# Kernel tuning notes

Hardware: AMD Instinct MI355X
Metric: run time of the kernel (lower is better)

Reference implementation:

```python
import jax, jax.numpy as jnp
import numpy as np

N_NODES = 100000
N_EDGES = 1600000
N_GRAPHS = 256
NODE = 64
EDGE = 64
GLOB = 64
HID = 64


def _lin_init(key, fan_in, fan_out):
    kw, kb = jax.random.split(key)
    bound = 1.0 / np.sqrt(fan_in)
    W = jax.random.uniform(kw, (fan_in, fan_out), minval=-bound, maxval=bound, dtype=jnp.float32)
    b = jax.random.uniform(kb, (fan_out,), minval=-bound, maxval=bound, dtype=jnp.float32)
    return W, b


def setup_inputs() -> dict:
    key = jax.random.key(0)
    ks = jax.random.split(key, 9)
    x = jax.random.normal(ks[0], (N_NODES, NODE), dtype=jnp.float32)
    edge_index = jax.random.randint(ks[1], (2, N_EDGES), 0, N_NODES, dtype=jnp.int32)
    edge_attr = jax.random.normal(ks[2], (N_EDGES, EDGE), dtype=jnp.float32)
    u = jax.random.normal(ks[3], (N_GRAPHS, GLOB), dtype=jnp.float32)
    batch = jnp.sort(jax.random.randint(ks[4], (N_NODES,), 0, N_GRAPHS, dtype=jnp.int32))
    W1a, b1a = _lin_init(ks[5], NODE + EDGE, HID)
    W1b, b1b = _lin_init(ks[6], HID, HID)
    W2a, b2a = _lin_init(ks[7], NODE + HID + GLOB, HID)
    W2b, b2b = _lin_init(ks[8], HID, NODE)
    return {"x": x, "edge_index": edge_index, "edge_attr": edge_attr, "u": u,
            "batch": batch, "W1a": W1a, "b1a": b1a, "W1b": W1b, "b1b": b1b,
            "W2a": W2a, "b2a": b2a, "W2b": W2b, "b2b": b2b}


def reference(x, edge_index, edge_attr, u, batch, W1a, b1a, W1b, b1b, W2a, b2a, W2b, b2b):
    row, col = edge_index[0], edge_index[1]
    # gather source node feats + edge feats -> [E, node+edge]
    out = jnp.concatenate([x[row], edge_attr], axis=1)
    out = jax.nn.selu(out @ W1a + b1a) @ W1b + b1b  # node_mlp_1 -> [E, HID]
    # scatter_mean into destination nodes
    summed = jax.ops.segment_sum(out, col, num_segments=x.shape[0])
    counts = jax.ops.segment_sum(jnp.ones((out.shape[0],), out.dtype), col, num_segments=x.shape[0])
    mean = summed / jnp.maximum(counts, 1.0)[:, None]
    h = jnp.concatenate([x, mean, u[batch]], axis=1)  # [N, node+HID+glob]
    return jax.nn.selu(h @ W2a + b2a) @ W2b + b2b
```

## Files before the change

### kernel.cpp

```cpp
#include <hip/hip_runtime.h>

#define NN 100000
#define NE 1600000
#define NT_E (NE / 16)
#define NT_N ((NN + 15) / 16)

typedef __attribute__((ext_vector_type(8))) short short8;
typedef __attribute__((ext_vector_type(4))) float f32x4;

__device__ __forceinline__ short f2b(float x) {
    unsigned u = __builtin_bit_cast(unsigned, x);
    u = (u + 0x7FFFu + ((u >> 16) & 1u)) >> 16;
    return (short)u;
}
__device__ __forceinline__ float b2f(unsigned short b) {
    return __builtin_bit_cast(float, (unsigned)b << 16);
}

__device__ __forceinline__ float selu_f(float x) {
    const float scale = 1.0507009873554805f;
    const float asc   = 1.7580993408473766f;
    return x > 0.f ? scale * x : asc * (__expf(x) - 1.f);
}

__device__ __forceinline__ short8 pack8(const float* __restrict__ p) {
    const f32x4 a = *reinterpret_cast<const f32x4*>(p);
    const f32x4 b = *reinterpret_cast<const f32x4*>(p + 4);
    short8 r;
#pragma unroll
    for (int j = 0; j < 4; ++j) { r[j] = f2b(a[j]); r[j + 4] = f2b(b[j]); }
    return r;
}

__device__ __forceinline__ short8 pack8nt(const float* __restrict__ p) {
    const f32x4 a = __builtin_nontemporal_load(reinterpret_cast<const f32x4*>(p));
    const f32x4 b = __builtin_nontemporal_load(reinterpret_cast<const f32x4*>(p + 4));
    short8 r;
#pragma unroll
    for (int j = 0; j < 4; ++j) { r[j] = f2b(a[j]); r[j + 4] = f2b(b[j]); }
    return r;
}

__device__ __forceinline__ short8 ld_frag(const unsigned short* __restrict__ base, int idx, int lane) {
    return *reinterpret_cast<const short8*>(base + ((size_t)idx * 64 + lane) * 8);
}

__device__ __forceinline__ f32x4 mm(short8 a, short8 b, f32x4 c) {
    return __builtin_amdgcn_mfma_f32_16x16x32_bf16(a, b, c, 0, 0, 0);
}

__global__ void frag_setup(const float* __restrict__ W1a, const float* __restrict__ W1b,
                           const float* __restrict__ W2a, const float* __restrict__ W2b,
                           unsigned short* __restrict__ fw) {
    const int lane = threadIdx.x;
    const int p = lane & 15, q = lane >> 4;
    const int f = blockIdx.x;
    const float* W; int idx; unsigned short* dst;
    if (f < 16)      { W = W1a; idx = f;      dst = fw; }
    else if (f < 24) { W = W1b; idx = f - 16; dst = fw + 16 * 512; }
    else if (f < 48) { W = W2a; idx = f - 24; dst = fw + 24 * 512; }
    else             { W = W2b; idx = f - 48; dst = fw + 48 * 512; }
    const int t = idx >> 2, n = idx & 3;
    const float* base = W + (t * 32 + q * 8) * 64 + n * 16 + p;
    unsigned short* o = dst + ((size_t)idx * 64 + lane) * 8;
#pragma unroll
    for (int j = 0; j < 8; ++j) o[j] = (unsigned short)f2b(base[j * 64]);
}

__global__ __launch_bounds__(256) void edge_kernel(
    const float* __restrict__ x, const int* __restrict__ row, const int* __restrict__ col,
    const float* __restrict__ ea,
    const unsigned short* __restrict__ fw1a, const float* __restrict__ b1a,
    const unsigned short* __restrict__ fw1b, const float* __restrict__ b1b,
    unsigned short* __restrict__ summed, float* __restrict__ counts)
{
    __shared__ __attribute__((aligned(16))) short hlds[4][16 * 72];
    const int lane = threadIdx.x & 63;
    const int wid  = threadIdx.x >> 6;
    const int p = lane & 15, q = lane >> 4;
    short* hl = hlds[wid];

    short8 B1[4][4], B2[2][4];
#pragma unroll
    for (int t = 0; t < 4; ++t)
#pragma unroll
        for (int n = 0; n < 4; ++n) B1[t][n] = ld_frag(fw1a, t * 4 + n, lane);
#pragma unroll
    for (int t = 0; t < 2; ++t)
#pragma unroll
        for (int n = 0; n < 4; ++n) B2[t][n] = ld_frag(fw1b, t * 4 + n, lane);
    float bias1[4], bias2[4];
#pragma unroll
    for (int n = 0; n < 4; ++n) { bias1[n] = b1a[n * 16 + p]; bias2[n] = b1b[n * 16 + p]; }

    const int tstride = gridDim.x * 4;
    int tile = blockIdx.x * 4 + wid;
    int rs = (tile < NT_E) ? row[tile * 16 + p] : 0;

    for (; tile < NT_E; tile += tstride) {
        const int e = tile * 16 + p;
        const float* xr = x + (size_t)rs * 64 + q * 8;
        const float* er = ea + (size_t)e * 64 + q * 8;
        short8 a0 = pack8(xr);
        short8 a1 = pack8(xr + 32);
        short8 a2 = pack8nt(er);
        short8 a3 = pack8nt(er + 32);

        const int tn = tile + tstride;
        const int rs_next = (tn < NT_E) ? row[tn * 16 + p] : 0;

        int cd[4];
#pragma unroll
        for (int i = 0; i < 4; ++i) cd[i] = col[tile * 16 + q * 4 + i];

        f32x4 acc[4];
#pragma unroll
        for (int n = 0; n < 4; ++n) acc[n] = (f32x4){0.f, 0.f, 0.f, 0.f};
#pragma unroll
        for (int n = 0; n < 4; ++n) {
            acc[n] = mm(a0, B1[0][n], acc[n]);
            acc[n] = mm(a1, B1[1][n], acc[n]);
            acc[n] = mm(a2, B1[2][n], acc[n]);
            acc[n] = mm(a3, B1[3][n], acc[n]);
        }
#pragma unroll
        for (int n = 0; n < 4; ++n)
#pragma unroll
            for (int i = 0; i < 4; ++i)
                hl[(q * 4 + i) * 72 + n * 16 + p] = f2b(selu_f(acc[n][i] + bias1[n]));

        short8 h0 = *reinterpret_cast<const short8*>(hl + p * 72 + q * 8);
        short8 h1 = *reinterpret_cast<const short8*>(hl + p * 72 + 32 + q * 8);

        f32x4 acc2[4];
#pragma unroll
        for (int n = 0; n < 4; ++n) acc2[n] = (f32x4){0.f, 0.f, 0.f, 0.f};
#pragma unroll
        for (int n = 0; n < 4; ++n) {
            acc2[n] = mm(h0, B2[0][n], acc2[n]);
            acc2[n] = mm(h1, B2[1][n], acc2[n]);
        }

#pragma unroll
        for (int n = 0; n < 4; ++n)
#pragma unroll
            for (int i = 0; i < 4; ++i) {
                const float v = acc2[n][i] + bias2[n];
                const float o = __shfl_xor(v, 1);
                if (!(p & 1)) {
                    unsigned pk = ((unsigned)(unsigned short)f2b(o) << 16) |
                                  (unsigned)(unsigned short)f2b(v);
                    unsigned long long addr =
                        (unsigned long long)(summed + (size_t)cd[i] * 64 + n * 16 + p);
                    asm volatile("global_atomic_pk_add_bf16 %0, %1, off"
                                 :: "v"(addr), "v"(pk) : "memory");
                }
            }
        if (lane < 16) unsafeAtomicAdd(&counts[col[e]], 1.0f);
        rs = rs_next;
    }
}

__global__ __launch_bounds__(256) void node_kernel(
    const float* __restrict__ x, const float* __restrict__ u, const int* __restrict__ batch,
    const unsigned short* __restrict__ summed, const float* __restrict__ counts,
    const unsigned short* __restrict__ fw2a, const float* __restrict__ b2a,
    const unsigned short* __restrict__ fw2b, const float* __restrict__ b2b,
    float* __restrict__ out)
{
    __shared__ __attribute__((aligned(16))) short hlds[4][16 * 72];
    const int lane = threadIdx.x & 63;
    const int wid  = threadIdx.x >> 6;
    const int p = lane & 15, q = lane >> 4;
    short* hl = hlds[wid];

    short8 BA[6][4], BB[2][4];
#pragma unroll
    for (int t = 0; t < 6; ++t)
#pragma unroll
        for (int n = 0; n < 4; ++n) BA[t][n] = ld_frag(fw2a, t * 4 + n, lane);
#pragma unroll
    for (int t = 0; t < 2; ++t)
#pragma unroll
        for (int n = 0; n < 4; ++n) BB[t][n] = ld_frag(fw2b, t * 4 + n, lane);
    float bias1[4], bias2[4];
#pragma unroll
    for (int n = 0; n < 4; ++n) { bias1[n] = b2a[n * 16 + p]; bias2[n] = b2b[n * 16 + p]; }

    const int tstride = gridDim.x * 4;
    for (int tile = blockIdx.x * 4 + wid; tile < NT_N; tile += tstride) {
        const int v = tile * 16 + p;
        const float* xr = x + (size_t)v * 64 + q * 8;
        short8 a0 = pack8(xr);
        short8 a1 = pack8(xr + 32);

        const float rc = 1.f / fmaxf(counts[v], 1.f);
        const unsigned short* sr = summed + (size_t)v * 64 + q * 8;
        short8 s0 = *reinterpret_cast<const short8*>(sr);
        short8 s1 = *reinterpret_cast<const short8*>(sr + 32);
        short8 a2, a3;
#pragma unroll
        for (int j = 0; j < 8; ++j) {
            a2[j] = f2b(b2f((unsigned short)s0[j]) * rc);
            a3[j] = f2b(b2f((unsigned short)s1[j]) * rc);
        }
        const int g = batch[v];
        const float* ur = u + (size_t)g * 64 + q * 8;
        short8 a4 = pack8(ur);
        short8 a5 = pack8(ur + 32);

        f32x4 acc[4];
#pragma unroll
        for (int n = 0; n < 4; ++n) acc[n] = (f32x4){0.f, 0.f, 0.f, 0.f};
#pragma unroll
        for (int n = 0; n < 4; ++n) {
            acc[n] = mm(a0, BA[0][n], acc[n]);
            acc[n] = mm(a1, BA[1][n], acc[n]);
            acc[n] = mm(a2, BA[2][n], acc[n]);
            acc[n] = mm(a3, BA[3][n], acc[n]);
            acc[n] = mm(a4, BA[4][n], acc[n]);
            acc[n] = mm(a5, BA[5][n], acc[n]);
        }
#pragma unroll
        for (int n = 0; n < 4; ++n)
#pragma unroll
            for (int i = 0; i < 4; ++i)
                hl[(q * 4 + i) * 72 + n * 16 + p] = f2b(selu_f(acc[n][i] + bias1[n]));

        short8 h0 = *reinterpret_cast<const short8*>(hl + p * 72 + q * 8);
        short8 h1 = *reinterpret_cast<const short8*>(hl + p * 72 + 32 + q * 8);

        f32x4 acc2[4];
#pragma unroll
        for (int n = 0; n < 4; ++n) acc2[n] = (f32x4){0.f, 0.f, 0.f, 0.f};
#pragma unroll
        for (int n = 0; n < 4; ++n) {
            acc2[n] = mm(h0, BB[0][n], acc2[n]);
            acc2[n] = mm(h1, BB[1][n], acc2[n]);
        }
#pragma unroll
        for (int n = 0; n < 4; ++n)
#pragma unroll
            for (int i = 0; i < 4; ++i)
                out[((size_t)tile * 16 + q * 4 + i) * 64 + n * 16 + p] = acc2[n][i] + bias2[n];
    }
}

extern "C" void kernel_launch(void* const* d_in, const int* in_sizes, int n_in,
                              void* d_out, int out_size, void* d_ws, size_t ws_size,
                              hipStream_t stream) {
    const float* x     = (const float*)d_in[0];
    const int*   ei    = (const int*)d_in[1];
    const float* ea    = (const float*)d_in[2];
    const float* u     = (const float*)d_in[3];
    const int*   batch = (const int*)d_in[4];
    const float* W1a   = (const float*)d_in[5];
    const float* b1a   = (const float*)d_in[6];
    const float* W1b   = (const float*)d_in[7];
    const float* b1b   = (const float*)d_in[8];
    const float* W2a   = (const float*)d_in[9];
    const float* b2a   = (const float*)d_in[10];
    const float* W2b   = (const float*)d_in[11];
    const float* b2b   = (const float*)d_in[12];
    float* out = (float*)d_out;

    unsigned short* summed = (unsigned short*)d_ws;
    float* counts = (float*)((char*)d_ws + (size_t)NN * 64 * 2);
    unsigned short* fw = (unsigned short*)((char*)d_ws + 13200000);
    const unsigned short* fw1a = fw;
    const unsigned short* fw1b = fw + 16 * 512;
    const unsigned short* fw2a = fw + 24 * 512;
    const unsigned short* fw2b = fw + 48 * 512;

    hipMemsetAsync(d_ws, 0, 13200000, stream);
    frag_setup<<<56, 64, 0, stream>>>(W1a, W1b, W2a, W2b, fw);

    const int* row = ei;
    const int* col = ei + NE;
    edge_kernel<<<1024, 256, 0, stream>>>(x, row, col, ea, fw1a, b1a, fw1b, b1b, summed, counts);
    node_kernel<<<1024, 256, 0, stream>>>(x, u, batch, summed, counts, fw2a, b2a, fw2b, b2b, out);
}
```

Baseline: 908.9 us.

## Replace atomic scatter with CSR gather and move second edge linear past mean

Builds a CSR by destination node (histogram, three-pass scan, atomic scatter of edge ids). Each wave then gathers its incoming edges, computes the first linear and SELU, and averages the activations in registers, writing a bf16 mean per node. Because the mean is linear, the second edge-MLP layer (W1b) is applied once per node in the node kernel, with its bias kept only for nodes that have edges. This removes the bf16 atomic adds and a quarter of the per-edge MMA work, at the cost of several extra preprocessing kernels, random gathers of edge_attr through the payload, and uneven per-node work (padded 16-edge tiles).

```diff
diff --git a/kernel.cpp b/kernel.cpp
--- a/kernel.cpp
+++ b/kernel.cpp
@@ -2,8 +2,8 @@
 
 #define NN 100000
 #define NE 1600000
-#define NT_E (NE / 16)
-#define NT_N ((NN + 15) / 16)
+#define NT_N (NN / 16)
+#define NBLK_SCAN 98
 
 typedef __attribute__((ext_vector_type(8))) short short8;
 typedef __attribute__((ext_vector_type(4))) float f32x4;
@@ -12,9 +12,6 @@
     unsigned u = __builtin_bit_cast(unsigned, x);
     u = (u + 0x7FFFu + ((u >> 16) & 1u)) >> 16;
     return (short)u;
-}
-__device__ __forceinline__ float b2f(unsigned short b) {
-    return __builtin_bit_cast(float, (unsigned)b << 16);
 }
 
 __device__ __forceinline__ float selu_f(float x) {
@@ -67,103 +64,136 @@
     for (int j = 0; j < 8; ++j) o[j] = (unsigned short)f2b(base[j * 64]);
 }
 
-__global__ __launch_bounds__(256) void edge_kernel(
-    const float* __restrict__ x, const int* __restrict__ row, const int* __restrict__ col,
-    const float* __restrict__ ea,
+__global__ void hist_kernel(const int* __restrict__ col, int* __restrict__ counts) {
+    int i = blockIdx.x * blockDim.x + threadIdx.x;
+    const int stride = gridDim.x * blockDim.x;
+    for (; i < NE; i += stride) atomicAdd(&counts[col[i]], 1);
+}
+
+__global__ __launch_bounds__(1024) void scanA(const int* __restrict__ counts,
+                                              int* __restrict__ starts, int* __restrict__ btot) {
+    __shared__ int sh[1024];
+    const int tid = threadIdx.x;
+    const int i = blockIdx.x * 1024 + tid;
+    const int v = (i < NN) ? counts[i] : 0;
+    sh[tid] = v; __syncthreads();
+#pragma unroll
+    for (int off = 1; off < 1024; off <<= 1) {
+        int t = (tid >= off) ? sh[tid - off] : 0;
+        __syncthreads();
+        sh[tid] += t; __syncthreads();
+    }
+    starts[i] = sh[tid] - v;
+    if (tid == 1023) btot[blockIdx.x] = sh[1023];
+}
+
+__global__ __launch_bounds__(128) void scanB(const int* __restrict__ btot, int* __restrict__ boff) {
+    __shared__ int sh[128];
+    const int tid = threadIdx.x;
+    const int v = (tid < NBLK_SCAN) ? btot[tid] : 0;
+    sh[tid] = v; __syncthreads();
+#pragma unroll
+    for (int off = 1; off < 128; off <<= 1) {
+        int t = (tid >= off) ? sh[tid - off] : 0;
+        __syncthreads();
+        sh[tid] += t; __syncthreads();
+    }
+    if (tid < NBLK_SCAN) boff[tid] = sh[tid] - v;
+}
+
+__global__ __launch_bounds__(1024) void scanC(int* __restrict__ starts, const int* __restrict__ boff,
+                                              int* __restrict__ cursor) {
+    const int i = blockIdx.x * 1024 + threadIdx.x;
+    const int s = starts[i] + boff[blockIdx.x];
+    starts[i] = s;
+    if (i < NN) cursor[i] = s;
+}
+
+__global__ void scatter_kernel(const int* __restrict__ col, int* __restrict__ cursor,
+                               int* __restrict__ payload) {
+    int i = blockIdx.x * blockDim.x + threadIdx.x;
+    const int stride = gridDim.x * blockDim.x;
+    for (; i < NE; i += stride) {
+        const int c = col[i];
+        const int pos = atomicAdd(&cursor[c], 1);
+        payload[pos] = i;
+    }
+}
+
+__global__ __launch_bounds__(256) void edge_gather(
+    const float* __restrict__ x, const int* __restrict__ row, const float* __restrict__ ea,
+    const int* __restrict__ starts, const int* __restrict__ payload,
     const unsigned short* __restrict__ fw1a, const float* __restrict__ b1a,
-    const unsigned short* __restrict__ fw1b, const float* __restrict__ b1b,
-    unsigned short* __restrict__ summed, float* __restrict__ counts)
+    unsigned short* __restrict__ hmean)
 {
-    __shared__ __attribute__((aligned(16))) short hlds[4][16 * 72];
     const int lane = threadIdx.x & 63;
     const int wid  = threadIdx.x >> 6;
     const int p = lane & 15, q = lane >> 4;
-    short* hl = hlds[wid];
-
-    short8 B1[4][4], B2[2][4];
+
+    short8 B1[4][4];
 #pragma unroll
     for (int t = 0; t < 4; ++t)
 #pragma unroll
         for (int n = 0; n < 4; ++n) B1[t][n] = ld_frag(fw1a, t * 4 + n, lane);
-#pragma unroll
-    for (int t = 0; t < 2; ++t)
-#pragma unroll
-        for (int n = 0; n < 4; ++n) B2[t][n] = ld_frag(fw1b, t * 4 + n, lane);
-    float bias1[4], bias2[4];
-#pragma unroll
-    for (int n = 0; n < 4; ++n) { bias1[n] = b1a[n * 16 + p]; bias2[n] = b1b[n * 16 + p]; }
-
-    const int tstride = gridDim.x * 4;
-    int tile = blockIdx.x * 4 + wid;
-    int rs = (tile < NT_E) ? row[tile * 16 + p] : 0;
-
-    for (; tile < NT_E; tile += tstride) {
-        const int e = tile * 16 + p;
-        const float* xr = x + (size_t)rs * 64 + q * 8;
-        const float* er = ea + (size_t)e * 64 + q * 8;
-        short8 a0 = pack8(xr);
-        short8 a1 = pack8(xr + 32);
-        short8 a2 = pack8nt(er);
-        short8 a3 = pack8nt(er + 32);
-
-        const int tn = tile + tstride;
-        const int rs_next = (tn < NT_E) ? row[tn * 16 + p] : 0;
-
-        int cd[4];
-#pragma unroll
-        for (int i = 0; i < 4; ++i) cd[i] = col[tile * 16 + q * 4 + i];
-
-        f32x4 acc[4];
-#pragma unroll
-        for (int n = 0; n < 4; ++n) acc[n] = (f32x4){0.f, 0.f, 0.f, 0.f};
+    float bias1[4];
+#pragma unroll
+    for (int n = 0; n < 4; ++n) bias1[n] = b1a[n * 16 + p];
+
+    const int nwave = gridDim.x * 4;
+    for (int v = blockIdx.x * 4 + wid; v < NN; v += nwave) {
+        const int s0 = starts[v];
+        const int k  = starts[v + 1] - s0;
+        float hsum[4] = {0.f, 0.f, 0.f, 0.f};
+        if (k > 0) {
+            const int ntile = (k + 15) >> 4;
+            for (int t = 0; t < ntile; ++t) {
+                const int slot = t * 16 + p;
+                const int sc = slot < k ? slot : k - 1;
+                const int e  = payload[s0 + sc];
+                const int rs = row[e];
+                const float* xr = x + (size_t)rs * 64 + q * 8;
+                const float* er = ea + (size_t)e * 64 + q * 8;
+                short8 a0 = pack8(xr);
+                short8 a1 = pack8(xr + 32);
+                short8 a2 = pack8nt(er);
+                short8 a3 = pack8nt(er + 32);
+
+                f32x4 acc[4];
+#pragma unroll
+                for (int n = 0; n < 4; ++n) acc[n] = (f32x4){0.f, 0.f, 0.f, 0.f};
+#pragma unroll
+                for (int n = 0; n < 4; ++n) {
+                    acc[n] = mm(a0, B1[0][n], acc[n]);
+                    acc[n] = mm(a1, B1[1][n], acc[n]);
+                    acc[n] = mm(a2, B1[2][n], acc[n]);
+                    acc[n] = mm(a3, B1[3][n], acc[n]);
+                }
+                const int rbase = t * 16 + q * 4;
+#pragma unroll
+                for (int n = 0; n < 4; ++n)
+#pragma unroll
+                    for (int i = 0; i < 4; ++i)
+                        if (rbase + i < k) hsum[n] += selu_f(acc[n][i] + bias1[n]);
+            }
+        }
 #pragma unroll
         for (int n = 0; n < 4; ++n) {
-            acc[n] = mm(a0, B1[0][n], acc[n]);
-            acc[n] = mm(a1, B1[1][n], acc[n]);
-            acc[n] = mm(a2, B1[2][n], acc[n]);
-            acc[n] = mm(a3, B1[3][n], acc[n]);
-        }
-#pragma unroll
-        for (int n = 0; n < 4; ++n)
-#pragma unroll
-            for (int i = 0; i < 4; ++i)
-                hl[(q * 4 + i) * 72 + n * 16 + p] = f2b(selu_f(acc[n][i] + bias1[n]));
-
-        short8 h0 = *reinterpret_cast<const short8*>(hl + p * 72 + q * 8);
-        short8 h1 = *reinterpret_cast<const short8*>(hl + p * 72 + 32 + q * 8);
-
-        f32x4 acc2[4];
-#pragma unroll
-        for (int n = 0; n < 4; ++n) acc2[n] = (f32x4){0.f, 0.f, 0.f, 0.f};
-#pragma unroll
-        for (int n = 0; n < 4; ++n) {
-            acc2[n] = mm(h0, B2[0][n], acc2[n]);
-            acc2[n] = mm(h1, B2[1][n], acc2[n]);
-        }
-
-#pragma unroll
-        for (int n = 0; n < 4; ++n)
-#pragma unroll
-            for (int i = 0; i < 4; ++i) {
-                const float v = acc2[n][i] + bias2[n];
-                const float o = __shfl_xor(v, 1);
-                if (!(p & 1)) {
-                    unsigned pk = ((unsigned)(unsigned short)f2b(o) << 16) |
-                                  (unsigned)(unsigned short)f2b(v);
-                    unsigned long long addr =
-                        (unsigned long long)(summed + (size_t)cd[i] * 64 + n * 16 + p);
-                    asm volatile("global_atomic_pk_add_bf16 %0, %1, off"
-                                 :: "v"(addr), "v"(pk) : "memory");
-                }
-            }
-        if (lane < 16) unsafeAtomicAdd(&counts[col[e]], 1.0f);
-        rs = rs_next;
+            hsum[n] += __shfl_xor(hsum[n], 16);
+            hsum[n] += __shfl_xor(hsum[n], 32);
+        }
+        const float rk = (k > 0) ? 1.f / (float)k : 0.f;
+        if (q == 0) {
+#pragma unroll
+            for (int n = 0; n < 4; ++n)
+                hmean[(size_t)v * 64 + n * 16 + p] = (unsigned short)f2b(hsum[n] * rk);
+        }
     }
 }
 
 __global__ __launch_bounds__(256) void node_kernel(
     const float* __restrict__ x, const float* __restrict__ u, const int* __restrict__ batch,
-    const unsigned short* __restrict__ summed, const float* __restrict__ counts,
+    const unsigned short* __restrict__ hmean, const int* __restrict__ starts,
+    const unsigned short* __restrict__ fw1b, const float* __restrict__ b1b,
     const unsigned short* __restrict__ fw2a, const float* __restrict__ b2a,
     const unsigned short* __restrict__ fw2b, const float* __restrict__ b2b,
     float* __restrict__ out)
@@ -174,7 +204,11 @@
     const int p = lane & 15, q = lane >> 4;
     short* hl = hlds[wid];
 
-    short8 BA[6][4], BB[2][4];
+    short8 BM[2][4], BA[6][4], BB[2][4];
+#pragma unroll
+    for (int t = 0; t < 2; ++t)
+#pragma unroll
+        for (int n = 0; n < 4; ++n) BM[t][n] = ld_frag(fw1b, t * 4 + n, lane);
 #pragma unroll
     for (int t = 0; t < 6; ++t)
 #pragma unroll
@@ -183,27 +217,45 @@
     for (int t = 0; t < 2; ++t)
 #pragma unroll
         for (int n = 0; n < 4; ++n) BB[t][n] = ld_frag(fw2b, t * 4 + n, lane);
-    float bias1[4], bias2[4];
-#pragma unroll
-    for (int n = 0; n < 4; ++n) { bias1[n] = b2a[n * 16 + p]; bias2[n] = b2b[n * 16 + p]; }
+    float biasm[4], bias1[4], bias2[4];
+#pragma unroll
+    for (int n = 0; n < 4; ++n) {
+        biasm[n] = b1b[n * 16 + p];
+        bias1[n] = b2a[n * 16 + p];
+        bias2[n] = b2b[n * 16 + p];
+    }
 
     const int tstride = gridDim.x * 4;
     for (int tile = blockIdx.x * 4 + wid; tile < NT_N; tile += tstride) {
         const int v = tile * 16 + p;
+        const unsigned short* hr = hmean + (size_t)v * 64 + q * 8;
+        short8 m0 = *reinterpret_cast<const short8*>(hr);
+        short8 m1 = *reinterpret_cast<const short8*>(hr + 32);
+        f32x4 mac[4];
+#pragma unroll
+        for (int n = 0; n < 4; ++n) mac[n] = (f32x4){0.f, 0.f, 0.f, 0.f};
+#pragma unroll
+        for (int n = 0; n < 4; ++n) {
+            mac[n] = mm(m0, BM[0][n], mac[n]);
+            mac[n] = mm(m1, BM[1][n], mac[n]);
+        }
+        const int vr = tile * 16 + q * 4;
+        int sA[5];
+#pragma unroll
+        for (int j = 0; j < 5; ++j) sA[j] = starts[vr + j];
+#pragma unroll
+        for (int i = 0; i < 4; ++i) {
+            const bool nz = sA[i + 1] > sA[i];
+#pragma unroll
+            for (int n = 0; n < 4; ++n)
+                hl[(q * 4 + i) * 72 + n * 16 + p] = f2b(nz ? mac[n][i] + biasm[n] : 0.f);
+        }
+        short8 a2 = *reinterpret_cast<const short8*>(hl + p * 72 + q * 8);
+        short8 a3 = *reinterpret_cast<const short8*>(hl + p * 72 + 32 + q * 8);
+
         const float* xr = x + (size_t)v * 64 + q * 8;
         short8 a0 = pack8(xr);
         short8 a1 = pack8(xr + 32);
-
-        const float rc = 1.f / fmaxf(counts[v], 1.f);
-        const unsigned short* sr = summed + (size_t)v * 64 + q * 8;
-        short8 s0 = *reinterpret_cast<const short8*>(sr);
-        short8 s1 = *reinterpret_cast<const short8*>(sr + 32);
-        short8 a2, a3;
-#pragma unroll
-        for (int j = 0; j < 8; ++j) {
-            a2[j] = f2b(b2f((unsigned short)s0[j]) * rc);
-            a3[j] = f2b(b2f((unsigned short)s1[j]) * rc);
-        }
         const int g = batch[v];
         const float* ur = u + (size_t)g * 64 + q * 8;
         short8 a4 = pack8(ur);
@@ -264,19 +316,29 @@
     const float* b2b   = (const float*)d_in[12];
     float* out = (float*)d_out;
 
-    unsigned short* summed = (unsigned short*)d_ws;
-    float* counts = (float*)((char*)d_ws + (size_t)NN * 64 * 2);
-    unsigned short* fw = (unsigned short*)((char*)d_ws + 13200000);
-    const unsigned short* fw1a = fw;
-    const unsigned short* fw1b = fw + 16 * 512;
-    const unsigned short* fw2a = fw + 24 * 512;
-    const unsigned short* fw2b = fw + 48 * 512;
-
-    hipMemsetAsync(d_ws, 0, 13200000, stream);
-    frag_setup<<<56, 64, 0, stream>>>(W1a, W1b, W2a, W2b, fw);
+    char* ws = (char*)d_ws;
+    int*            payload = (int*)(ws + 0);
+    unsigned short* hmean   = (unsigned short*)(ws + 6400000);
+    int*            starts  = (int*)(ws + 19200000);
+    int*            cursor  = (int*)(ws + 19601408);
+    int*            counts  = (int*)(ws + 20001408);
+    int*            btot    = (int*)(ws + 20401408);
+    int*            boff    = (int*)(ws + 20401920);
+    unsigned short* fw      = (unsigned short*)(ws + 20402432);
 
     const int* row = ei;
     const int* col = ei + NE;
-    edge_kernel<<<1024, 256, 0, stream>>>(x, row, col, ea, fw1a, b1a, fw1b, b1b, summed, counts);
-    node_kernel<<<1024, 256, 0, stream>>>(x, u, batch, summed, counts, fw2a, b2a, fw2b, b2b, out);
-}
+
+    hipMemsetAsync(counts, 0, NN * sizeof(int), stream);
+    frag_setup<<<56, 64, 0, stream>>>(W1a, W1b, W2a, W2b, fw);
+    hist_kernel<<<1024, 256, 0, stream>>>(col, counts);
+    scanA<<<NBLK_SCAN, 1024, 0, stream>>>(counts, starts, btot);
+    scanB<<<1, 128, 0, stream>>>(btot, boff);
+    scanC<<<NBLK_SCAN, 1024, 0, stream>>>(starts, boff, cursor);
+    scatter_kernel<<<1024, 256, 0, stream>>>(col, cursor, payload);
+    edge_gather<<<2048, 256, 0, stream>>>(x, row, ea, starts, payload,
+                                          fw, b1a, hmean);
+    node_kernel<<<1024, 256, 0, stream>>>(x, u, batch, hmean, starts,
+                                          fw + 16 * 512, b1b, fw + 24 * 512, b2a,
+                                          fw + 48 * 512, b2b, out);
+}
```

New measurement: 893.8 us. About the same (-1.7%).
